# Kernel optimization log

Measured on AMD Instinct MI355X. Metric: run time of the kernel, lower is better.

Reference implementation:

```python
import jax, jax.numpy as jnp
import numpy as np
from jax import lax

B, S, MAX_WORD = 64, 40, 25
L = S * MAX_WORD            # 1000 tokens
D_IN, D = 768, 256
G = 6                       # lda_group_num
KW, KS = 5, 3               # word / sentence conv kernel sizes


def _conv1d(x, W, b, pad):
    # x: (B, Cin, L), W: (Cout, Cin, K) -> (B, Cout, L) ('same' via explicit pad)
    y = lax.conv_general_dilated(x, W, window_strides=(1,), padding=[(pad, pad)],
                                 dimension_numbers=('NCH', 'OIH', 'NCH'))
    return y + b[None, :, None]


def _mha(x, Wq, bq, Wk, bk, Wv, bv, Wo, bo):
    # single-head self-attention; x: (batch, seq, D)
    q = x @ Wq + bq
    k = x @ Wk + bk
    v = x @ Wv + bv
    scores = jnp.einsum('bqd,bkd->bqk', q, k) / jnp.sqrt(jnp.asarray(D, x.dtype))
    attn = jax.nn.softmax(scores, axis=-1)
    out = jnp.einsum('bqk,bkd->bqd', attn, v)
    return out @ Wo + bo


def setup_inputs() -> dict:
    key = jax.random.key(0)
    ks = jax.random.split(key, 32)
    s = 0.05
    p = lambda k, shape: jax.random.normal(k, shape, jnp.float32) * s
    x = jax.random.normal(ks[0], (B, D_IN, L), jnp.float32)
    lda = jax.random.randint(ks[1], (B, S), 0, G)
    # guarantee each group non-empty per row (original would NaN on empty groups)
    lda = lda.at[:, :G].set(jnp.broadcast_to(jnp.arange(G), (B, G)))
    inp = {'x': x, 'lda_groups': lda,
           'Wc_w': p(ks[2], (D, D_IN, KW)), 'bc_w': p(ks[3], (D,)),
           'Wq_w': p(ks[4], (D, D)), 'bq_w': p(ks[5], (D,)),
           'Wk_w': p(ks[6], (D, D)), 'bk_w': p(ks[7], (D,)),
           'Wv_w': p(ks[8], (D, D)), 'bv_w': p(ks[9], (D,)),
           'Wo_w': p(ks[10], (D, D)), 'bo_w': p(ks[11], (D,)),
           'Wc_s': p(ks[12], (D, D, KS)), 'bc_s': p(ks[13], (D,)),
           'Wq_s': p(ks[14], (D, D)), 'bq_s': p(ks[15], (D,)),
           'Wk_s': p(ks[16], (D, D)), 'bk_s': p(ks[17], (D,)),
           'Wv_s': p(ks[18], (D, D)), 'bv_s': p(ks[19], (D,)),
           'Wo_s': p(ks[20], (D, D)), 'bo_s': p(ks[21], (D,)),
           'Wq_a': p(ks[22], (D, D)), 'bq_a': p(ks[23], (D,)),
           'Wk_a': p(ks[24], (D, D)), 'bk_a': p(ks[25], (D,)),
           'Wv_a': p(ks[26], (D, D)), 'bv_a': p(ks[27], (D,)),
           'Wo_a': p(ks[28], (D, D)), 'bo_a': p(ks[29], (D,))}
    return inp


def reference(x, lda_groups, Wc_w, bc_w, Wq_w, bq_w, Wk_w, bk_w, Wv_w, bv_w, Wo_w, bo_w,
              Wc_s, bc_s, Wq_s, bq_s, Wk_s, bk_s, Wv_s, bv_s, Wo_s, bo_s,
              Wq_a, bq_a, Wk_a, bk_a, Wv_a, bv_a, Wo_a, bo_a):
    # word-level CNN (dropout = identity in eval) + attention gate
    h = jax.nn.relu(_conv1d(x, Wc_w, bc_w, (KW - 1) // 2))      # (B, D, L)
    h = jnp.transpose(h, (0, 2, 1))                              # (B, L, D)
    h = h * _mha(h, Wq_w, bq_w, Wk_w, bk_w, Wv_w, bv_w, Wo_w, bo_w)
    # word_level_mean: contiguous blocks of MAX_WORD words -> sentence vectors
    h = h.reshape(B, S, MAX_WORD, D).mean(axis=2)                # (B, S, D)
    # sentence-level CNN
    h = jnp.transpose(h, (0, 2, 1))
    h = jax.nn.relu(_conv1d(h, Wc_s, bc_s, (KS - 1) // 2))
    h = jnp.transpose(h, (0, 2, 1))                              # (B, S, D)
    # sentence attention: torch MHA has batch_first=False but gets (B,S,D),
    # i.e. it attends over the batch axis with S as batch -> transpose
    ht = jnp.transpose(h, (1, 0, 2))
    a = jnp.transpose(_mha(ht, Wq_s, bq_s, Wk_s, bk_s, Wv_s, bv_s, Wo_s, bo_s), (1, 0, 2))
    h = h * a
    # aspect_level_mean (faithful to the original bug): per (batch, group) the
    # mean is a SCALAR over selected sentences AND all channels, broadcast to D
    mask = (lda_groups[:, :, None] == jnp.arange(G)[None, None, :]).astype(h.dtype)  # (B,S,G)
    gsum = jnp.einsum('bs,bsg->bg', h.sum(-1), mask)
    cnt = mask.sum(axis=1) * D
    ha = jnp.broadcast_to((gsum / cnt)[:, :, None], (B, G, D))   # (B, G, D)
    # aspect attention applied twice with the SAME params; same batch_first quirk
    for _ in range(2):
        hat = jnp.transpose(ha, (1, 0, 2))
        a = jnp.transpose(_mha(hat, Wq_a, bq_a, Wk_a, bk_a, Wv_a, bv_a, Wo_a, bo_a), (1, 0, 2))
        ha = ha * a
    return ha
```

## Files before the change

### kernel.cpp

```cpp
#include <hip/hip_runtime.h>
#include <hip/hip_bf16.h>


typedef unsigned short u16;
typedef __attribute__((ext_vector_type(8))) short bf16x8;
typedef __attribute__((ext_vector_type(4))) float f32x4;

__device__ __forceinline__ float bf2f(u16 u) {
  union { float f; unsigned int i; } x; x.i = ((unsigned int)u) << 16; return x.f;
}
__device__ __forceinline__ u16 f2bf(float f) {
  union { float f; unsigned int i; } x; x.f = f;
  unsigned int i = x.i;
  i += 0x7FFFu + ((i >> 16) & 1u);
  return (u16)(i >> 16);
}
__device__ __forceinline__ void gload16(const u16* g, u16* l) {
  __builtin_amdgcn_global_load_lds(
      (const __attribute__((address_space(1))) unsigned int*)g,
      (__attribute__((address_space(3))) unsigned int*)l, 16, 0, 0);
}

__global__ __launch_bounds__(256) void prep_weights_kernel(
    const float* __restrict__ Wc_w, const float* __restrict__ Wq_w,
    const float* __restrict__ Wk_w, const float* __restrict__ Wv_w,
    const float* __restrict__ Wo_w, const float* __restrict__ bq_w,
    const float* __restrict__ bk_w, const float* __restrict__ bv_w,
    const float* __restrict__ Wc_s,
    u16* __restrict__ WtT, u16* __restrict__ WqkvT, u16* __restrict__ WoT,
    float* __restrict__ bqkv, float* __restrict__ Wts)
{
  int idx = blockIdx.x * 256 + threadIdx.x;
  if (idx < 983040) {
    int n = idx / 3840, kk = idx % 3840;
    int k = kk / 768, c = kk % 768;
    WtT[idx] = f2bf(Wc_w[n * 3840 + c * 5 + k]);
  }
  if (idx < 196608) {
    int n = idx >> 8, kd = idx & 255;
    float v = (n < 256) ? Wq_w[kd * 256 + n]
            : (n < 512) ? Wk_w[kd * 256 + (n - 256)]
                        : Wv_w[kd * 256 + (n - 512)];
    WqkvT[idx] = f2bf(v);
  }
  if (idx < 65536) {
    int n = idx >> 8, kd = idx & 255;
    WoT[idx] = f2bf(Wo_w[kd * 256 + n]);
  }
  if (idx < 768) {
    bqkv[idx] = (idx < 256) ? bq_w[idx] : (idx < 512) ? bk_w[idx - 256] : bv_w[idx - 512];
  }
  if (idx < 196608) {
    int kk = idx >> 8, d = idx & 255;
    int k = kk >> 8, dc = kk & 255;
    Wts[idx] = Wc_s[d * 768 + dc * 3 + k];
  }
}

__global__ __launch_bounds__(256) void zero_pad_kernel(u16* __restrict__ xT)
{
  int idx = blockIdx.x * 256 + threadIdx.x;
  if (idx >= 1376256) return;
  int b = idx / 21504, rem = idx % 21504;
  int rowi = rem / 768, c = rem % 768;
  int row = (rowi < 2) ? rowi : (1000 + rowi);
  xT[((size_t)b * 1028 + row) * 768 + c] = (u16)0;
}

__global__ __launch_bounds__(256) void transpose_x_kernel(const float* __restrict__ x,
                                                          u16* __restrict__ xT)
{
  __shared__ float lds[64][65];
  int t = threadIdx.x, tr = t >> 6, tc = t & 63;
  int bid = blockIdx.x;
  int b = bid / 192, rem = bid % 192;
  int c0 = (rem / 16) * 64, l0 = (rem % 16) * 64;
  #pragma unroll
  for (int i = 0; i < 16; i++) {
    int rr = i * 4 + tr;
    int l = l0 + tc;
    lds[rr][tc] = (l < 1000) ? x[((size_t)b * 768 + c0 + rr) * 1000 + l] : 0.f;
  }
  __syncthreads();
  #pragma unroll
  for (int i = 0; i < 16; i++) {
    int rr = i * 4 + tr;
    int l = l0 + rr;
    if (l < 1000) xT[((size_t)b * 1028 + 2 + l) * 768 + c0 + tc] = f2bf(lds[tc][rr]);
  }
}

__global__ __launch_bounds__(256) void transpose_v_kernel(const u16* __restrict__ qkv,
                                                          u16* __restrict__ vT)
{
  __shared__ u16 lds[64][65];
  int t = threadIdx.x, tr = t >> 6, tc = t & 63;
  int bid = blockIdx.x;
  int b = bid >> 6, rem = bid & 63;
  int d0 = (rem >> 4) * 64, kv0 = (rem & 15) * 64;
  #pragma unroll
  for (int i = 0; i < 16; i++) {
    int rr = i * 4 + tr;
    int kv = kv0 + rr;
    lds[rr][tc] = (kv < 1000) ? qkv[((size_t)(b * 1000) + kv) * 768 + 512 + d0 + tc] : (u16)0;
  }
  __syncthreads();
  #pragma unroll
  for (int i = 0; i < 16; i++) {
    int rr = i * 4 + tr;
    vT[((size_t)(b * 256) + d0 + rr) * 1024 + kv0 + tc] = lds[tc][rr];
  }
}

template<bool CONV, bool RELU>
__global__ __launch_bounds__(256, 3) void gemm_bf16_kernel(
    const u16* __restrict__ A, const u16* __restrict__ Bt,
    const float* __restrict__ bias, u16* __restrict__ C,
    int lda, int K, int nk, int ntiles, int ldc)
{
  __shared__ u16 Alds[64 * 64];
  __shared__ u16 Blds[256 * 64];
  int t = threadIdx.x;
  int wave = t >> 6, lane = t & 63;
  int l15 = lane & 15, l4 = lane >> 4;
  int mt = blockIdx.x / ntiles, nt = blockIdx.x % ntiles;
  int wn = wave * 64;

  unsigned int aoff[2]; int aldsoff[2];
  #pragma unroll
  for (int i = 0; i < 2; i++) {
    int c = wave * 2 + i;
    int lr = c * 8 + (lane >> 3);
    int ss = (lane & 7) ^ (lr & 7);
    int gm = mt * 64 + lr;
    unsigned int base;
    if (CONV) base = (unsigned int)((gm >> 10) * 789504 + (gm & 1023) * 768);
    else      base = (unsigned int)gm * (unsigned int)lda;
    aoff[i] = base + (unsigned int)(ss * 8);
    aldsoff[i] = c * 512;
  }
  unsigned int boff[8]; int bldsoff[8];
  #pragma unroll
  for (int i = 0; i < 8; i++) {
    int c = wave * 8 + i;
    int lr = c * 8 + (lane >> 3);
    int ss = (lane & 7) ^ (lr & 7);
    boff[i] = (unsigned int)(nt * 256 + lr) * (unsigned int)K + (unsigned int)(ss * 8);
    bldsoff[i] = c * 512;
  }

  f32x4 acc[4][4];
  #pragma unroll
  for (int mf = 0; mf < 4; mf++)
    #pragma unroll
    for (int nf = 0; nf < 4; nf++) acc[mf][nf] = f32x4{0.f, 0.f, 0.f, 0.f};

  for (int ks = 0; ks < nk; ks++) {
    unsigned int ko = (unsigned int)ks * 64u;
    #pragma unroll
    for (int i = 0; i < 2; i++) gload16(A + aoff[i] + ko, &Alds[aldsoff[i]]);
    #pragma unroll
    for (int i = 0; i < 8; i++) gload16(Bt + boff[i] + ko, &Blds[bldsoff[i]]);
    __syncthreads();
    #pragma unroll
    for (int kc = 0; kc < 2; kc++) {
      int q = kc * 4 + l4;
      bf16x8 af[4], bfr[4];
      #pragma unroll
      for (int mf = 0; mf < 4; mf++) {
        int r = mf * 16 + l15;
        af[mf] = *(const bf16x8*)(&Alds[r * 64 + ((q ^ (r & 7)) * 8)]);
      }
      #pragma unroll
      for (int nf = 0; nf < 4; nf++) {
        int rb = wn + nf * 16 + l15;
        bfr[nf] = *(const bf16x8*)(&Blds[rb * 64 + ((q ^ (rb & 7)) * 8)]);
      }
      #pragma unroll
      for (int mf = 0; mf < 4; mf++)
        #pragma unroll
        for (int nf = 0; nf < 4; nf++)
          acc[mf][nf] = __builtin_amdgcn_mfma_f32_16x16x32_bf16(af[mf], bfr[nf], acc[mf][nf], 0, 0, 0);
    }
    __syncthreads();
  }
  float bv[4];
  #pragma unroll
  for (int nf = 0; nf < 4; nf++) bv[nf] = bias[nt * 256 + wn + nf * 16 + l15];
  #pragma unroll
  for (int mf = 0; mf < 4; mf++) {
    #pragma unroll
    for (int r = 0; r < 4; r++) {
      int rowl = mf * 16 + l4 * 4 + r;
      int gm = mt * 64 + rowl;
      size_t orow; bool ok = true;
      if (CONV) { int bb = gm >> 10, ll = gm & 1023; ok = (ll < 1000); orow = (size_t)bb * 1000 + ll; }
      else orow = (size_t)gm;
      if (ok) {
        #pragma unroll
        for (int nf = 0; nf < 4; nf++) {
          float v = acc[mf][nf][r] + bv[nf];
          if (RELU) v = fmaxf(v, 0.f);
          C[orow * ldc + nt * 256 + wn + nf * 16 + l15] = f2bf(v);
        }
      }
    }
  }
}

__global__ __launch_bounds__(256, 3) void flash_kernel(
    const u16* __restrict__ qkv, const u16* __restrict__ vT, u16* __restrict__ ctx)
{
  __shared__ u16 Klds[32 * 256];
  __shared__ u16 Vlds[256 * 32];
  __shared__ u16 Plds[4 * 640];
  int t = threadIdx.x, wave = t >> 6, lane = t & 63;
  int l15 = lane & 15, l4 = lane >> 4;
  int b = blockIdx.x >> 4, qt = blockIdx.x & 15;

  int qrow = qt * 64 + wave * 16 + l15;
  const u16* qp = qkv + ((size_t)(b * 1000) + qrow) * 768;
  bf16x8 qreg[8];
  #pragma unroll
  for (int kk = 0; kk < 8; kk++) qreg[kk] = *(const bf16x8*)(qp + kk * 32 + l4 * 8);

  f32x4 acc[16];
  #pragma unroll
  for (int df = 0; df < 16; df++) acc[df] = f32x4{0.f, 0.f, 0.f, 0.f};
  float tsum[4] = {0.f, 0.f, 0.f, 0.f};

  const u16* ksrc[4]; int kdst[4];
  const u16* vsrc[4]; int vdst[4];
  #pragma unroll
  for (int i = 0; i < 4; i++) {
    int c = i * 256 + t;
    int kr = c >> 5, kslot = c & 31;
    ksrc[i] = qkv + ((size_t)(b * 1000 + kr)) * 768 + 256 + kslot * 8;
    kdst[i] = kr * 256 + ((kslot ^ (kr & 7)) * 8);
    int vd = c >> 2, vslot = c & 3;
    vsrc[i] = vT + ((size_t)(b * 256 + vd)) * 1024 + vslot * 8;
    vdst[i] = vd * 32 + ((vslot ^ (vd & 3)) * 8);
  }
  bf16x8 kreg[4], vreg[4];
  #pragma unroll
  for (int i = 0; i < 4; i++) { kreg[i] = *(const bf16x8*)ksrc[i]; vreg[i] = *(const bf16x8*)vsrc[i]; }

  u16* pl = &Plds[wave * 640];

  for (int tile = 0; tile < 32; tile++) {
    __syncthreads();
    #pragma unroll
    for (int i = 0; i < 4; i++) {
      *(bf16x8*)(&Klds[kdst[i]]) = kreg[i];
      *(bf16x8*)(&Vlds[vdst[i]]) = vreg[i];
    }
    __syncthreads();
    if (tile + 1 < 32) {
      #pragma unroll
      for (int i = 0; i < 4; i++) {
        kreg[i] = *(const bf16x8*)(ksrc[i] + (size_t)(tile + 1) * 32 * 768);
        vreg[i] = *(const bf16x8*)(vsrc[i] + (tile + 1) * 32);
      }
    }
    f32x4 s[2];
    #pragma unroll
    for (int cf = 0; cf < 2; cf++) {
      s[cf] = f32x4{0.f, 0.f, 0.f, 0.f};
      int kr = cf * 16 + l15;
      #pragma unroll
      for (int kk = 0; kk < 8; kk++) {
        bf16x8 kf = *(const bf16x8*)(&Klds[kr * 256 + (((kk * 4 + l4) ^ (kr & 7)) * 8)]);
        s[cf] = __builtin_amdgcn_mfma_f32_16x16x32_bf16(qreg[kk], kf, s[cf], 0, 0, 0);
      }
    }
    int colb = tile * 32;
    float pv[2][4];
    #pragma unroll
    for (int r = 0; r < 4; r++) {
      float s0 = s[0][r] * 0.0625f;
      float s1 = s[1][r] * 0.0625f;
      if (colb + l15 >= 1000)      s0 = -1e30f;
      if (colb + 16 + l15 >= 1000) s1 = -1e30f;
      float p0 = __expf(s0 - 20.f);
      float p1 = __expf(s1 - 20.f);
      tsum[r] += p0 + p1;
      pv[0][r] = p0; pv[1][r] = p1;
    }
    #pragma unroll
    for (int cf = 0; cf < 2; cf++)
      #pragma unroll
      for (int r = 0; r < 4; r++)
        pl[(l4 * 4 + r) * 40 + cf * 16 + l15] = f2bf(pv[cf][r]);
    bf16x8 pa = *(const bf16x8*)(&pl[l15 * 40 + l4 * 8]);
    #pragma unroll
    for (int df = 0; df < 16; df++) {
      int d = df * 16 + l15;
      bf16x8 vf = *(const bf16x8*)(&Vlds[d * 32 + ((l4 ^ (d & 3)) * 8)]);
      acc[df] = __builtin_amdgcn_mfma_f32_16x16x32_bf16(pa, vf, acc[df], 0, 0, 0);
    }
  }
  #pragma unroll
  for (int r = 0; r < 4; r++) {
    float ts = tsum[r];
    #pragma unroll
    for (int mk = 1; mk < 16; mk <<= 1) ts += __shfl_xor(ts, mk, 16);
    tsum[r] = ts;
  }
  int orow0 = qt * 64 + wave * 16 + l4 * 4;
  #pragma unroll
  for (int r = 0; r < 4; r++) {
    int orow = orow0 + r;
    if (orow < 1000) {
      float inv = 1.0f / tsum[r];
      size_t base = ((size_t)(b * 1000) + orow) * 256;
      #pragma unroll
      for (int df = 0; df < 16; df++)
        ctx[base + df * 16 + l15] = f2bf(acc[df][r] * inv);
    }
  }
}

__global__ __launch_bounds__(256) void gate_mean_kernel(const u16* __restrict__ h,
                                                        const u16* __restrict__ ao,
                                                        u16* __restrict__ hmpad)
{
  int r = blockIdx.x, t = threadIdx.x;
  int b = r / 40, s = r % 40;
  size_t base = ((size_t)b * 1000 + s * 25) * 256 + t;
  float acc = 0.f;
  #pragma unroll 5
  for (int w = 0; w < 25; w++) acc += bf2f(h[base + (size_t)w * 256]) * bf2f(ao[base + (size_t)w * 256]);
  hmpad[((size_t)b * 42 + 1 + s) * 256 + t] = f2bf(acc * 0.04f);
}

__global__ __launch_bounds__(256) void sent_conv_kernel(const u16* __restrict__ hmpad,
                                                        const float* __restrict__ Wts,
                                                        const float* __restrict__ bc_s,
                                                        float* __restrict__ hs)
{
  __shared__ float alds[10 * 256];
  int t = threadIdx.x;
  int b = blockIdx.x / 5, s0 = (blockIdx.x % 5) * 8;
  #pragma unroll
  for (int i = 0; i < 10; i++)
    alds[i * 256 + t] = bf2f(hmpad[((size_t)b * 42 + s0 + i) * 256 + t]);
  __syncthreads();
  float acc[8]; float bv = bc_s[t];
  #pragma unroll
  for (int j = 0; j < 8; j++) acc[j] = bv;
  for (int kk = 0; kk < 768; kk++) {
    float w = Wts[(size_t)kk * 256 + t];
    #pragma unroll
    for (int j = 0; j < 8; j++) acc[j] += alds[j * 256 + kk] * w;
  }
  #pragma unroll
  for (int j = 0; j < 8; j++)
    hs[((size_t)b * 40 + s0 + j) * 256 + t] = fmaxf(acc[j], 0.f);
}

__global__ __launch_bounds__(256) void proj3_kernel(
    const float* __restrict__ A,
    const float* __restrict__ Wq, const float* __restrict__ bq,
    const float* __restrict__ Wk, const float* __restrict__ bk,
    const float* __restrict__ Wv, const float* __restrict__ bv,
    float* __restrict__ oq, float* __restrict__ okk, float* __restrict__ ov,
    int nb, int GS)
{
  __shared__ float alds[8 * 256];
  int sel = blockIdx.x / nb;
  int m0 = (blockIdx.x % nb) * 8;
  const float* W = (sel == 0) ? Wq : (sel == 1) ? Wk : Wv;
  const float* bias_ = (sel == 0) ? bq : (sel == 1) ? bk : bv;
  float* out = (sel == 0) ? oq : (sel == 1) ? okk : ov;
  int t = threadIdx.x;
  #pragma unroll
  for (int i = 0; i < 8; i++) {
    int r = m0 + i;
    int src = (r & 63) * GS + (r >> 6);
    alds[i * 256 + t] = A[(size_t)src * 256 + t];
  }
  __syncthreads();
  float acc[8]; float bv_ = bias_[t];
  #pragma unroll
  for (int i = 0; i < 8; i++) acc[i] = bv_;
  for (int k = 0; k < 256; k++) {
    float w = W[(size_t)k * 256 + t];
    #pragma unroll
    for (int i = 0; i < 8; i++) acc[i] += alds[i * 256 + k] * w;
  }
  #pragma unroll
  for (int i = 0; i < 8; i++) out[((size_t)m0 + i) * 256 + t] = acc[i];
}

__global__ __launch_bounds__(256) void attn_fused_kernel(
    const float* __restrict__ q, const float* __restrict__ k,
    const float* __restrict__ v, const float* __restrict__ Wo,
    const float* __restrict__ bo, const float* __restrict__ gate_src,
    float* __restrict__ out, int GS)
{
  __shared__ float pbuf[4][64];
  __shared__ float pvals[64];
  __shared__ float obuf[256];
  int r = blockIdx.x;
  int bb = r >> 6, i = r & 63;
  int t = threadIdx.x, tj = t & 63, part = t >> 6;
  const float* qrow = q + (size_t)r * 256 + part * 64;
  const float* krow = k + ((size_t)(bb * 64) + tj) * 256 + part * 64;
  float pp = 0.f;
  #pragma unroll 16
  for (int kk = 0; kk < 64; kk++) pp += qrow[kk] * krow[kk];
  pbuf[part][tj] = pp;
  __syncthreads();
  if (t < 64) {
    float s = (pbuf[0][t] + pbuf[1][t] + pbuf[2][t] + pbuf[3][t]) * 0.0625f;
    float mx = s;
    #pragma unroll
    for (int mk = 1; mk < 64; mk <<= 1) mx = fmaxf(mx, __shfl_xor(mx, mk, 64));
    float p = __expf(s - mx);
    float sm = p;
    #pragma unroll
    for (int mk = 1; mk < 64; mk <<= 1) sm += __shfl_xor(sm, mk, 64);
    pvals[t] = p / sm;
  }
  __syncthreads();
  float acc = 0.f;
  const float* vb = v + (size_t)(bb * 64) * 256 + t;
  for (int j = 0; j < 64; j++) acc += pvals[j] * vb[(size_t)j * 256];
  obuf[t] = acc;
  __syncthreads();
  float o = bo[t];
  for (int kk = 0; kk < 256; kk++) o += obuf[kk] * Wo[(size_t)kk * 256 + t];
  size_t gi = (size_t)i * GS + bb;
  out[gi * 256 + t] = gate_src[gi * 256 + t] * o;
}

__global__ __launch_bounds__(256) void aspect_mean_kernel(const float* __restrict__ h2,
                                                          const int* __restrict__ ldaG,
                                                          float* __restrict__ ha0)
{
  __shared__ float partbuf[6][256];
  __shared__ int ldas[40];
  __shared__ float gval[6];
  int b = blockIdx.x, t = threadIdx.x;
  if (t < 40) ldas[t] = ldaG[b * 40 + t];
  __syncthreads();
  float part[6] = {0, 0, 0, 0, 0, 0};
  for (int idx = t; idx < 10240; idx += 256) {
    int s = idx >> 8, d = idx & 255;
    float v = h2[((size_t)b * 40 + s) * 256 + d];
    int g = ldas[s];
    #pragma unroll
    for (int gg = 0; gg < 6; gg++) if (g == gg) part[gg] += v;
  }
  #pragma unroll
  for (int g = 0; g < 6; g++) partbuf[g][t] = part[g];
  __syncthreads();
  if (t < 6) {
    float ssum = 0.f;
    for (int i = 0; i < 256; i++) ssum += partbuf[t][i];
    int cnt = 0;
    for (int s = 0; s < 40; s++) cnt += (ldas[s] == t) ? 1 : 0;
    gval[t] = ssum / ((float)cnt * 256.0f);
  }
  __syncthreads();
  #pragma unroll
  for (int g = 0; g < 6; g++) ha0[((size_t)b * 6 + g) * 256 + t] = gval[g];
}

extern "C" void kernel_launch(void* const* d_in, const int* in_sizes, int n_in,
                              void* d_out, int out_size, void* d_ws, size_t ws_size,
                              hipStream_t stream) {
  (void)in_sizes; (void)n_in; (void)out_size; (void)ws_size;
  const float* x    = (const float*)d_in[0];
  const int*   ldaG = (const int*)d_in[1];
  const float* Wc_w = (const float*)d_in[2];
  const float* bc_w = (const float*)d_in[3];
  const float* Wq_w = (const float*)d_in[4];
  const float* bq_w = (const float*)d_in[5];
  const float* Wk_w = (const float*)d_in[6];
  const float* bk_w = (const float*)d_in[7];
  const float* Wv_w = (const float*)d_in[8];
  const float* bv_w = (const float*)d_in[9];
  const float* Wo_w = (const float*)d_in[10];
  const float* bo_w = (const float*)d_in[11];
  const float* Wc_s = (const float*)d_in[12];
  const float* bc_s = (const float*)d_in[13];
  const float* Wq_s = (const float*)d_in[14];
  const float* bq_s = (const float*)d_in[15];
  const float* Wk_s = (const float*)d_in[16];
  const float* bk_s = (const float*)d_in[17];
  const float* Wv_s = (const float*)d_in[18];
  const float* bv_s = (const float*)d_in[19];
  const float* Wo_s = (const float*)d_in[20];
  const float* bo_s = (const float*)d_in[21];
  const float* Wq_a = (const float*)d_in[22];
  const float* bq_a = (const float*)d_in[23];
  const float* Wk_a = (const float*)d_in[24];
  const float* bk_a = (const float*)d_in[25];
  const float* Wv_a = (const float*)d_in[26];
  const float* bv_a = (const float*)d_in[27];
  const float* Wo_a = (const float*)d_in[28];
  const float* bo_a = (const float*)d_in[29];

  char* ws = (char*)d_ws;
  u16*  xT    = (u16*)(ws + 0);
  u16*  qkvb  = (u16*)(ws + 0);
  u16*  attno = (u16*)(ws + 0);
  u16*  WtT   = (u16*)(ws + 101056512ULL);
  u16*  WqkvT = (u16*)(ws + 103022592ULL);
  u16*  WoT   = (u16*)(ws + 103415808ULL);
  float* bqkv = (float*)(ws + 103546880ULL);
  float* Wts  = (float*)(ws + 103549952ULL);
  u16*  h     = (u16*)(ws + 104336384ULL);
  u16*  ctx   = (u16*)(ws + 137104384ULL);
  u16*  vT    = (u16*)(ws + 169872384ULL);
  u16*  hmpad = (u16*)(ws + 203426816ULL);
  float* hs   = (float*)(ws + 204803072ULL);
  float* sq   = (float*)(ws + 207424512ULL);
  float* sk   = (float*)(ws + 210045952ULL);
  float* sv   = (float*)(ws + 212667392ULL);
  float* h2   = (float*)(ws + 215288832ULL);
  float* ha0  = (float*)(ws + 217910272ULL);
  float* aq   = (float*)(ws + 218303488ULL);
  float* ak   = (float*)(ws + 218696704ULL);
  float* av   = (float*)(ws + 219089920ULL);
  float* ha1  = (float*)(ws + 219483136ULL);

  hipMemsetAsync(hmpad, 0, 1376256ULL, stream);
  zero_pad_kernel<<<5376, 256, 0, stream>>>(xT);

  prep_weights_kernel<<<3840, 256, 0, stream>>>(Wc_w, Wq_w, Wk_w, Wv_w, Wo_w,
                                                bq_w, bk_w, bv_w, Wc_s,
                                                WtT, WqkvT, WoT, bqkv, Wts);
  transpose_x_kernel<<<12288, 256, 0, stream>>>(x, xT);
  gemm_bf16_kernel<true, true><<<1024, 256, 0, stream>>>(xT, WtT, bc_w, h, 768, 3840, 60, 1, 256);
  gemm_bf16_kernel<false, false><<<3000, 256, 0, stream>>>(h, WqkvT, bqkv, qkvb, 256, 256, 4, 3, 768);
  transpose_v_kernel<<<4096, 256, 0, stream>>>(qkvb, vT);
  flash_kernel<<<1024, 256, 0, stream>>>(qkvb, vT, ctx);
  gemm_bf16_kernel<false, false><<<1000, 256, 0, stream>>>(ctx, WoT, bo_w, attno, 256, 256, 4, 1, 256);
  gate_mean_kernel<<<2560, 256, 0, stream>>>(h, attno, hmpad);
  sent_conv_kernel<<<320, 256, 0, stream>>>(hmpad, Wts, bc_s, hs);
  proj3_kernel<<<960, 256, 0, stream>>>(hs, Wq_s, bq_s, Wk_s, bk_s, Wv_s, bv_s,
                                        sq, sk, sv, 320, 40);
  attn_fused_kernel<<<2560, 256, 0, stream>>>(sq, sk, sv, Wo_s, bo_s, hs, h2, 40);
  aspect_mean_kernel<<<64, 256, 0, stream>>>(h2, ldaG, ha0);

  const float* hacur = ha0;
  for (int it = 0; it < 2; it++) {
    proj3_kernel<<<144, 256, 0, stream>>>(hacur, Wq_a, bq_a, Wk_a, bk_a, Wv_a, bv_a,
                                          aq, ak, av, 48, 6);
    float* dst = (it == 0) ? ha1 : (float*)d_out;
    attn_fused_kernel<<<384, 256, 0, stream>>>(aq, ak, av, Wo_a, bo_a, hacur, dst, 6);
    hacur = dst;
  }
}
```

Measured before the change: 691.0 us.

## Double-buffer GEMM LDS tiles and vectorize transpose and padding kernels

The bf16 GEMM now prefetches the next K tile into a second LDS buffer while computing on the current one, so global-to-LDS loads overlap with MFMA work. The launch bound drops from 3 to 2 blocks per CU to fit the doubled LDS. The x and v transpose kernels and the zero-pad kernel switch to vector loads and stores, cutting instruction count and improving coalescing. The risks are lower occupancy and reliance on the barrier to wait for the async LDS loads.

```diff
diff --git a/kernel.cpp b/kernel.cpp
--- a/kernel.cpp
+++ b/kernel.cpp
@@ -5,6 +5,8 @@
 typedef unsigned short u16;
 typedef __attribute__((ext_vector_type(8))) short bf16x8;
 typedef __attribute__((ext_vector_type(4))) float f32x4;
+typedef __attribute__((ext_vector_type(4))) unsigned short u16x4;
+typedef __attribute__((ext_vector_type(8))) unsigned short u16x8;
 
 __device__ __forceinline__ float bf2f(u16 u) {
   union { float f; unsigned int i; } x; x.i = ((unsigned int)u) << 16; return x.f;
@@ -59,34 +61,45 @@
 
 __global__ __launch_bounds__(256) void zero_pad_kernel(u16* __restrict__ xT)
 {
-  int idx = blockIdx.x * 256 + threadIdx.x;
-  if (idx >= 1376256) return;
-  int b = idx / 21504, rem = idx % 21504;
+  int c8 = blockIdx.x * 256 + threadIdx.x;
+  if (c8 >= 172032) return;
+  int e = c8 * 8;
+  int b = e / 21504, rem = e % 21504;
   int rowi = rem / 768, c = rem % 768;
   int row = (rowi < 2) ? rowi : (1000 + rowi);
-  xT[((size_t)b * 1028 + row) * 768 + c] = (u16)0;
+  u16x8 z = {0, 0, 0, 0, 0, 0, 0, 0};
+  *(u16x8*)&xT[((size_t)b * 1028 + row) * 768 + c] = z;
 }
 
 __global__ __launch_bounds__(256) void transpose_x_kernel(const float* __restrict__ x,
                                                           u16* __restrict__ xT)
 {
   __shared__ float lds[64][65];
-  int t = threadIdx.x, tr = t >> 6, tc = t & 63;
+  int t = threadIdx.x;
   int bid = blockIdx.x;
   int b = bid / 192, rem = bid % 192;
   int c0 = (rem / 16) * 64, l0 = (rem % 16) * 64;
-  #pragma unroll
-  for (int i = 0; i < 16; i++) {
-    int rr = i * 4 + tr;
-    int l = l0 + tc;
-    lds[rr][tc] = (l < 1000) ? x[((size_t)b * 768 + c0 + rr) * 1000 + l] : 0.f;
-  }
-  __syncthreads();
-  #pragma unroll
-  for (int i = 0; i < 16; i++) {
-    int rr = i * 4 + tr;
-    int l = l0 + rr;
-    if (l < 1000) xT[((size_t)b * 1028 + 2 + l) * 768 + c0 + tc] = f2bf(lds[tc][rr]);
+  int pr = t >> 4, plc = (t & 15) * 4;
+  #pragma unroll
+  for (int i = 0; i < 4; i++) {
+    int r = i * 16 + pr;
+    f32x4 v = {0.f, 0.f, 0.f, 0.f};
+    if (l0 + plc < 1000)
+      v = *(const f32x4*)&x[((size_t)b * 768 + c0 + r) * 1000 + l0 + plc];
+    lds[r][plc + 0] = v[0]; lds[r][plc + 1] = v[1];
+    lds[r][plc + 2] = v[2]; lds[r][plc + 3] = v[3];
+  }
+  __syncthreads();
+  int qr = t >> 3, qc = (t & 7) * 8;
+  #pragma unroll
+  for (int i = 0; i < 2; i++) {
+    int l = i * 32 + qr;
+    if (l0 + l < 1000) {
+      u16x8 o;
+      #pragma unroll
+      for (int j = 0; j < 8; j++) o[j] = f2bf(lds[qc + j][l]);
+      *(u16x8*)&xT[((size_t)b * 1028 + 2 + l0 + l) * 768 + c0 + qc] = o;
+    }
   }
 }
 
@@ -94,32 +107,40 @@
                                                           u16* __restrict__ vT)
 {
   __shared__ u16 lds[64][65];
-  int t = threadIdx.x, tr = t >> 6, tc = t & 63;
-  int bid = blockIdx.x;
-  int b = bid >> 6, rem = bid & 63;
+  int t = threadIdx.x;
+  int b = blockIdx.x >> 6, rem = blockIdx.x & 63;
   int d0 = (rem >> 4) * 64, kv0 = (rem & 15) * 64;
-  #pragma unroll
-  for (int i = 0; i < 16; i++) {
-    int rr = i * 4 + tr;
-    int kv = kv0 + rr;
-    lds[rr][tc] = (kv < 1000) ? qkv[((size_t)(b * 1000) + kv) * 768 + 512 + d0 + tc] : (u16)0;
-  }
-  __syncthreads();
-  #pragma unroll
-  for (int i = 0; i < 16; i++) {
-    int rr = i * 4 + tr;
-    vT[((size_t)(b * 256) + d0 + rr) * 1024 + kv0 + tc] = lds[tc][rr];
+  int pr = t >> 4, plc = (t & 15) * 4;
+  #pragma unroll
+  for (int i = 0; i < 4; i++) {
+    int kvl = i * 16 + pr;
+    int kv = kv0 + kvl;
+    u16x4 v = {0, 0, 0, 0};
+    if (kv < 1000)
+      v = *(const u16x4*)&qkv[((size_t)(b * 1000) + kv) * 768 + 512 + d0 + plc];
+    lds[kvl][plc + 0] = v[0]; lds[kvl][plc + 1] = v[1];
+    lds[kvl][plc + 2] = v[2]; lds[kvl][plc + 3] = v[3];
+  }
+  __syncthreads();
+  int qr = t >> 3, qc = (t & 7) * 8;
+  #pragma unroll
+  for (int i = 0; i < 2; i++) {
+    int d = i * 32 + qr;
+    u16x8 o;
+    #pragma unroll
+    for (int j = 0; j < 8; j++) o[j] = lds[qc + j][d];
+    *(u16x8*)&vT[((size_t)(b * 256) + d0 + d) * 1024 + kv0 + qc] = o;
   }
 }
 
 template<bool CONV, bool RELU>
-__global__ __launch_bounds__(256, 3) void gemm_bf16_kernel(
+__global__ __launch_bounds__(256, 2) void gemm_bf16_kernel(
     const u16* __restrict__ A, const u16* __restrict__ Bt,
     const float* __restrict__ bias, u16* __restrict__ C,
     int lda, int K, int nk, int ntiles, int ldc)
 {
-  __shared__ u16 Alds[64 * 64];
-  __shared__ u16 Blds[256 * 64];
+  __shared__ u16 Alds[2][64 * 64];
+  __shared__ u16 Blds[2][256 * 64];
   int t = threadIdx.x;
   int wave = t >> 6, lane = t & 63;
   int l15 = lane & 15, l4 = lane >> 4;
@@ -155,13 +176,23 @@
     #pragma unroll
     for (int nf = 0; nf < 4; nf++) acc[mf][nf] = f32x4{0.f, 0.f, 0.f, 0.f};
 
+  #pragma unroll
+  for (int i = 0; i < 2; i++) gload16(A + aoff[i], &Alds[0][aldsoff[i]]);
+  #pragma unroll
+  for (int i = 0; i < 8; i++) gload16(Bt + boff[i], &Blds[0][bldsoff[i]]);
+  __syncthreads();
+
+  int cur = 0;
   for (int ks = 0; ks < nk; ks++) {
-    unsigned int ko = (unsigned int)ks * 64u;
-    #pragma unroll
-    for (int i = 0; i < 2; i++) gload16(A + aoff[i] + ko, &Alds[aldsoff[i]]);
-    #pragma unroll
-    for (int i = 0; i < 8; i++) gload16(Bt + boff[i] + ko, &Blds[bldsoff[i]]);
-    __syncthreads();
+    if (ks + 1 < nk) {
+      unsigned int ko = (unsigned int)(ks + 1) * 64u;
+      #pragma unroll
+      for (int i = 0; i < 2; i++) gload16(A + aoff[i] + ko, &Alds[cur ^ 1][aldsoff[i]]);
+      #pragma unroll
+      for (int i = 0; i < 8; i++) gload16(Bt + boff[i] + ko, &Blds[cur ^ 1][bldsoff[i]]);
+    }
+    const u16* Ab = &Alds[cur][0];
+    const u16* Bb = &Blds[cur][0];
     #pragma unroll
     for (int kc = 0; kc < 2; kc++) {
       int q = kc * 4 + l4;
@@ -169,12 +200,12 @@
       #pragma unroll
       for (int mf = 0; mf < 4; mf++) {
         int r = mf * 16 + l15;
-        af[mf] = *(const bf16x8*)(&Alds[r * 64 + ((q ^ (r & 7)) * 8)]);
+        af[mf] = *(const bf16x8*)(&Ab[r * 64 + ((q ^ (r & 7)) * 8)]);
       }
       #pragma unroll
       for (int nf = 0; nf < 4; nf++) {
         int rb = wn + nf * 16 + l15;
-        bfr[nf] = *(const bf16x8*)(&Blds[rb * 64 + ((q ^ (rb & 7)) * 8)]);
+        bfr[nf] = *(const bf16x8*)(&Bb[rb * 64 + ((q ^ (rb & 7)) * 8)]);
       }
       #pragma unroll
       for (int mf = 0; mf < 4; mf++)
@@ -183,6 +214,7 @@
           acc[mf][nf] = __builtin_amdgcn_mfma_f32_16x16x32_bf16(af[mf], bfr[nf], acc[mf][nf], 0, 0, 0);
     }
     __syncthreads();
+    cur ^= 1;
   }
   float bv[4];
   #pragma unroll
@@ -527,7 +559,7 @@
   float* ha1  = (float*)(ws + 219483136ULL);
 
   hipMemsetAsync(hmpad, 0, 1376256ULL, stream);
-  zero_pad_kernel<<<5376, 256, 0, stream>>>(xT);
+  zero_pad_kernel<<<672, 256, 0, stream>>>(xT);
 
   prep_weights_kernel<<<3840, 256, 0, stream>>>(Wc_w, Wq_w, Wk_w, Wv_w, Wo_w,
                                                 bq_w, bk_w, bv_w, Wc_s,
```

Measured after the change: 705.2 us. +2.0%, slower.
